# Optimization experiments

Measured on AMD Instinct MI355X. Metric: run time of the kernel, lower is better.

Reference implementation:

```python
import jax, jax.numpy as jnp
import numpy as np

B, N, K, M = 4, 32768, 128, 1024
C_IN, C_OUT, C_ATT, H = 256, 256, 256, 8
G = 32  # GroupNorm groups
EPS = 1e-6


def heat_diffusion(x, mass, evals, evecs, t):
    # to_basis: evecs^T @ (mass * x)  -> [B,K,C]
    x_spec = jnp.einsum('bnk,bnc->bkc', evecs, x * mass[..., None])
    coefs = jnp.exp(-evals[..., None] * t[None, None, :])  # [B,K,C]
    # from_basis: evecs @ spec -> [B,N,C]
    return jnp.einsum('bnk,bkc->bnc', evecs, coefs * x_spec)


def setup_inputs() -> dict:
    key = jax.random.key(0)
    ks = jax.random.split(key, 16)
    x = jax.random.normal(ks[0], (B, N, C_IN), jnp.float32)
    mass = jax.random.uniform(ks[1], (B, N), jnp.float32, 0.1, 1.0)
    evals = jnp.sort(jax.random.uniform(ks[2], (B, K), jnp.float32, 0.0, 10.0), axis=-1)
    evecs = jax.random.normal(ks[3], (B, N, K), jnp.float32) / np.sqrt(N)
    # unique sorted farthest-point indices per mesh (equiv. to boolean mask with M True)
    far_idx = jnp.stack([jnp.sort(jax.random.permutation(jax.random.fold_in(ks[4], b), N)[:M])
                         for b in range(B)]).astype(jnp.int32)
    s = 1.0 / np.sqrt(C_IN)
    params = dict(
        diff_in_t=jnp.full((C_IN,), 0.01, jnp.float32),
        diff_out_t=jnp.full((C_OUT,), 0.01, jnp.float32),
        gn_w=jnp.ones((C_IN,), jnp.float32),
        gn_b=jnp.zeros((C_IN,), jnp.float32),
        Wq=jax.random.normal(ks[5], (C_IN, C_ATT), jnp.float32) * s,
        bq=jnp.zeros((C_ATT,), jnp.float32),
        Wk=jax.random.normal(ks[6], (C_IN, C_ATT), jnp.float32) * s,
        bk=jnp.zeros((C_ATT,), jnp.float32),
        Wv=jax.random.normal(ks[7], (C_IN, C_ATT), jnp.float32) * s,
        bv=jnp.zeros((C_ATT,), jnp.float32),
        Wo=jax.random.normal(ks[8], (C_ATT, C_OUT), jnp.float32) * s,
        bo=jnp.zeros((C_OUT,), jnp.float32),
        out_w=jnp.ones((C_OUT,), jnp.float32),
    )
    return dict(x=x, mass=mass, evals=evals, evecs=evecs, far_idx=far_idx, **params)


def reference(x, mass, evals, evecs, far_idx, diff_in_t, diff_out_t, gn_w, gn_b,
              Wq, bq, Wk, bk, Wv, bv, Wo, bo, out_w):
    # clamp (torch does this in-place under no_grad)
    diff_in_t = jnp.maximum(diff_in_t, 1e-8)
    diff_out_t = jnp.maximum(diff_out_t, 1e-8)
    out_w = jnp.maximum(out_w, 1e-8)

    x = heat_diffusion(x, mass, evals, evecs, diff_in_t)  # [B,N,C_IN]

    # masked gather of farthest points -> [B,M,C_IN]
    x_far = jnp.take_along_axis(x, far_idx[..., None], axis=1)

    # GroupNorm over (group-channels, points)
    xg = x_far.reshape(B, M, G, C_IN // G)
    mu = jnp.mean(xg, axis=(1, 3), keepdims=True)
    var = jnp.var(xg, axis=(1, 3), keepdims=True)
    xg = (xg - mu) * jax.lax.rsqrt(var + EPS)
    x_far = xg.reshape(B, M, C_IN) * gn_w + gn_b

    d = C_ATT // H
    q = (x_far @ Wq + bq).reshape(B, M, H, d)
    k = (x_far @ Wk + bk).reshape(B, M, H, d)
    v = (x_far @ Wv + bv).reshape(B, M, H, d)
    scores = jnp.einsum('bqhd,bkhd->bhqk', q, k) / np.sqrt(d)
    attn = jax.nn.softmax(scores, axis=-1)
    x_far = jnp.einsum('bhqk,bkhd->bqhd', attn, v).reshape(B, M, C_ATT)
    x_far = x_far @ Wo + bo  # [B,M,C_OUT]

    # scatter back into zeros at the farthest-point rows
    z = jnp.zeros((B, N, C_OUT), x.dtype)
    z = z.at[jnp.arange(B)[:, None], far_idx].set(x_far)

    out = heat_diffusion(z, mass, evals, evecs, diff_out_t)
    return out * out_w[None, None, :]
```

## Files before the change

### kernel.cpp

```cpp
#include <hip/hip_runtime.h>
#include <hip/hip_bf16.h>


#define Bn 4
#define Nn 32768
#define Kn 128
#define Cn 256
#define Mn 1024
#define Hn 8
#define Dn 32
#define NCH 64
#define MCH 16

typedef _Float16 f16;
typedef _Float16 f16x8 __attribute__((ext_vector_type(8)));
typedef float f32x4 __attribute__((ext_vector_type(4)));
typedef unsigned int u32;
typedef unsigned int u32x4 __attribute__((ext_vector_type(4)));

__device__ __forceinline__ void gload_lds16(const float* g, float* l) {
    __builtin_amdgcn_global_load_lds(
        (const __attribute__((address_space(1))) void*)g,
        (__attribute__((address_space(3))) void*)l, 16, 0, 0);
}

static __device__ __forceinline__ u32 packf16(f16 a, f16 b) {
    union { f16 h[2]; u32 u; } x;
    x.h[0] = a; x.h[1] = b;
    return x.u;
}

__global__ __launch_bounds__(512) void k_tobasis1(
    const float* __restrict__ x, const float* __restrict__ mass,
    const float* __restrict__ evecs, float* __restrict__ part)
{
    const int nch = blockIdx.x, b = blockIdx.z;
    const int n0 = nch * (Nn / NCH);
    const int t = threadIdx.x;
    const int lane = t & 63, w = t >> 6;
    const int lr = lane & 15, lg = lane >> 4;
    const int wm = (w & 1) * 64;
    const int wc = (w >> 1) * 64;

    __shared__ __align__(16) float evS[2][32][128];
    __shared__ __align__(16) float xS[2][32][256];
    __shared__ __align__(16) f16 evT[128][64];
    __shared__ __align__(16) f16 xT[256][64];
    __shared__ __align__(16) float massS[512];

    const size_t rb0 = (size_t)b * Nn + n0;
    const float* ebase = evecs + rb0 * Kn;
    const float* xbase = x + rb0 * Cn;

    f32x4 acc[4][4] = {};

    if (w < 2) gload_lds16(mass + rb0 + w * 256 + lane * 4, massS + w * 256);
#pragma unroll
    for (int ss = 0; ss < 2; ss++) {
        const float* eb = ebase + (size_t)ss * 32 * Kn;
        const float* xb = xbase + (size_t)ss * 32 * Cn;
#pragma unroll
        for (int iw = 0; iw < 2; iw++)
            gload_lds16(eb + (w * 2 + iw) * 256 + lane * 4, &evS[ss][0][0] + (w * 2 + iw) * 256);
#pragma unroll
        for (int iw = 0; iw < 4; iw++)
            gload_lds16(xb + (w * 4 + iw) * 256 + lane * 4, &xS[ss][0][0] + (w * 4 + iw) * 256);
    }

    for (int s = 0; s < 16; s++) {
        const int p = s & 1;
        if (s == 15) { asm volatile("s_waitcnt vmcnt(0)" ::: "memory"); }
        else         { asm volatile("s_waitcnt vmcnt(6)" ::: "memory"); }
        __builtin_amdgcn_sched_barrier(0);
        __builtin_amdgcn_s_barrier();

        {
            const int k = t & 127;
            const int g = t >> 7;
            f16x8 hv, lv;
#pragma unroll
            for (int r = 0; r < 8; r++) {
                const float f = evS[p][g * 8 + r][k];
                const f16 h = (f16)f;
                hv[r] = h;
                lv[r] = (f16)(f - (float)h);
            }
            *(f16x8*)&evT[k][((g) ^ (k & 7)) * 8] = hv;
            *(f16x8*)&evT[k][((4 + g) ^ (k & 7)) * 8] = lv;
        }
        {
            const int c = t & 255;
            const int g2 = t >> 8;
#pragma unroll
            for (int jj = 0; jj < 2; jj++) {
                const int ch = g2 * 2 + jj;
                f16x8 hv, lv;
#pragma unroll
                for (int r = 0; r < 8; r++) {
                    const int n = ch * 8 + r;
                    const float f = xS[p][n][c] * massS[s * 32 + n];
                    const f16 h = (f16)f;
                    hv[r] = h;
                    lv[r] = (f16)(f - (float)h);
                }
                *(f16x8*)&xT[c][((ch) ^ (c & 7)) * 8] = hv;
                *(f16x8*)&xT[c][((4 + ch) ^ (c & 7)) * 8] = lv;
            }
        }

        asm volatile("s_waitcnt lgkmcnt(0)" ::: "memory");
        __builtin_amdgcn_sched_barrier(0);
        __builtin_amdgcn_s_barrier();

        if (s + 2 < 16) {
            const float* eb = ebase + (size_t)(s + 2) * 32 * Kn;
            const float* xb = xbase + (size_t)(s + 2) * 32 * Cn;
#pragma unroll
            for (int iw = 0; iw < 2; iw++)
                gload_lds16(eb + (w * 2 + iw) * 256 + lane * 4, &evS[p][0][0] + (w * 2 + iw) * 256);
#pragma unroll
            for (int iw = 0; iw < 4; iw++)
                gload_lds16(xb + (w * 4 + iw) * 256 + lane * 4, &xS[p][0][0] + (w * 4 + iw) * 256);
        }

        f16x8 aH[4], aL[4], bH[4], bL[4];
#pragma unroll
        for (int i = 0; i < 4; i++) {
            const int rk = wm + i * 16 + lr;
            aH[i] = *(const f16x8*)&evT[rk][((lg) ^ (rk & 7)) * 8];
            aL[i] = *(const f16x8*)&evT[rk][((4 + lg) ^ (rk & 7)) * 8];
            const int rc = wc + i * 16 + lr;
            bH[i] = *(const f16x8*)&xT[rc][((lg) ^ (rc & 7)) * 8];
            bL[i] = *(const f16x8*)&xT[rc][((4 + lg) ^ (rc & 7)) * 8];
        }
#pragma unroll
        for (int i = 0; i < 4; i++)
#pragma unroll
            for (int j = 0; j < 4; j++) {
                acc[i][j] = __builtin_amdgcn_mfma_f32_16x16x32_f16(aH[i], bH[j], acc[i][j], 0, 0, 0);
                acc[i][j] = __builtin_amdgcn_mfma_f32_16x16x32_f16(aH[i], bL[j], acc[i][j], 0, 0, 0);
                acc[i][j] = __builtin_amdgcn_mfma_f32_16x16x32_f16(aL[i], bH[j], acc[i][j], 0, 0, 0);
            }
    }

    float* dst = part + ((size_t)b * NCH + nch) * (Kn * Cn);
#pragma unroll
    for (int i = 0; i < 4; i++)
#pragma unroll
        for (int j = 0; j < 4; j++) {
            const int m0 = wm + i * 16 + lg * 4;
            const int c = wc + j * 16 + lr;
#pragma unroll
            for (int r = 0; r < 4; r++)
                dst[(size_t)(m0 + r) * Cn + c] = acc[i][j][r];
        }
}

__global__ __launch_bounds__(256) void k_reduce(
    const float* __restrict__ part, int nchunks,
    const float* __restrict__ evals, const float* __restrict__ tvec,
    float* __restrict__ spec)
{
    const int b = blockIdx.x >> 7, k = blockIdx.x & 127, c = threadIdx.x;
    float ssum = 0.f;
    const float* p = part + ((size_t)b * nchunks * Kn + k) * Cn + c;
    for (int j = 0; j < nchunks; j++) ssum += p[(size_t)j * Kn * Cn];
    const float lam = evals[b * Kn + k];
    const float tt = fmaxf(tvec[c], 1e-8f);
    spec[((size_t)b * Kn + k) * Cn + c] = ssum * __expf(-lam * tt);
}

__global__ __launch_bounds__(256) void k_spectr(
    const float* __restrict__ spec, f16* __restrict__ sTh, f16* __restrict__ sTl)
{
    const int kc = blockIdx.x, b = blockIdx.y;
    const int t = threadIdx.x;
    __shared__ f16 lh[32][258];
    __shared__ f16 ll[32][258];
#pragma unroll 8
    for (int k2 = 0; k2 < 32; k2++) {
        const float f = spec[((size_t)b * Kn + kc * 32 + k2) * Cn + t];
        const f16 h = (f16)f;
        lh[k2][t] = h;
        ll[k2][t] = (f16)(f - (float)h);
    }
    __syncthreads();
    f16x8 vh[4], vl[4];
#pragma unroll
    for (int q = 0; q < 4; q++)
#pragma unroll
        for (int j = 0; j < 8; j++) { vh[q][j] = lh[q * 8 + j][t]; vl[q][j] = ll[q * 8 + j][t]; }
    f16* dh = sTh + ((size_t)b * 256 + t) * Kn + kc * 32;
    f16* dl = sTl + ((size_t)b * 256 + t) * Kn + kc * 32;
#pragma unroll
    for (int q = 0; q < 4; q++) {
        *(f16x8*)(dh + q * 8) = vh[q];
        *(f16x8*)(dl + q * 8) = vl[q];
    }
}

__global__ __launch_bounds__(128) void k_gather(
    const float* __restrict__ evecs, const float* __restrict__ mass,
    const int* __restrict__ far, float* __restrict__ evf, float* __restrict__ massf)
{
    const int row = blockIdx.x;
    const int b = row >> 10;
    const int idx = far[row];
    const int t = threadIdx.x;
    evf[(size_t)row * Kn + t] = evecs[((size_t)b * Nn + idx) * Kn + t];
    if (t == 0) massf[row] = mass[(size_t)b * Nn + idx];
}

struct G3 {
    const float* W[3];
    const float* bias[3];
    float* out[3];
};

template<int KD, bool PERB, bool MMASS>
__global__ __launch_bounds__(256) void k_gemm64(
    const float* __restrict__ X, G3 g, const float* __restrict__ massf)
{
    const int mt = blockIdx.x, ct = blockIdx.y, z = blockIdx.z;
    const int row0 = mt * 64, c0 = ct * 64;
    const int b = row0 >> 10;
    const float* Wp = g.W[z];
    const float* bias = g.bias[z];
    float* out = g.out[z];
    const size_t woff = PERB ? (size_t)b * KD * 256 : 0;

    __shared__ float xT[32][68];
    __shared__ float wl[32][64];
    const int t = threadIdx.x, tx = t & 15, ty = t >> 4;
    float acc[4][4] = {};

    for (int k0 = 0; k0 < KD; k0 += 32) {
        {
            const int m = t >> 2, cc0 = (t & 3) * 8;
            const float* xs = X + (size_t)(row0 + m) * KD + k0 + cc0;
            float4 a0 = *(const float4*)xs, a1 = *(const float4*)(xs + 4);
            xT[cc0 + 0][m] = a0.x; xT[cc0 + 1][m] = a0.y; xT[cc0 + 2][m] = a0.z; xT[cc0 + 3][m] = a0.w;
            xT[cc0 + 4][m] = a1.x; xT[cc0 + 5][m] = a1.y; xT[cc0 + 6][m] = a1.z; xT[cc0 + 7][m] = a1.w;
        }
        {
            const int cc = t >> 3, col = (t & 7) * 8;
            const float* wsrc = Wp + woff + (size_t)(k0 + cc) * 256 + c0 + col;
            float4 a0 = *(const float4*)wsrc, a1 = *(const float4*)(wsrc + 4);
            wl[cc][col + 0] = a0.x; wl[cc][col + 1] = a0.y; wl[cc][col + 2] = a0.z; wl[cc][col + 3] = a0.w;
            wl[cc][col + 4] = a1.x; wl[cc][col + 5] = a1.y; wl[cc][col + 6] = a1.z; wl[cc][col + 7] = a1.w;
        }
        __syncthreads();
#pragma unroll 8
        for (int cc = 0; cc < 32; cc++) {
            float4 xv = *(const float4*)&xT[cc][ty * 4];
            float4 wv = *(const float4*)&wl[cc][tx * 4];
            float xa[4] = {xv.x, xv.y, xv.z, xv.w};
            float wa[4] = {wv.x, wv.y, wv.z, wv.w};
#pragma unroll
            for (int i = 0; i < 4; i++)
#pragma unroll
                for (int j = 0; j < 4; j++) acc[i][j] += xa[i] * wa[j];
        }
        __syncthreads();
    }
    float bj[4] = {0.f, 0.f, 0.f, 0.f};
    if (bias) {
#pragma unroll
        for (int j = 0; j < 4; j++) bj[j] = bias[c0 + tx * 4 + j];
    }
#pragma unroll
    for (int i = 0; i < 4; i++) {
        const int row = row0 + ty * 4 + i;
        const float mm = MMASS ? massf[row] : 1.f;
        *(float4*)(out + (size_t)row * 256 + c0 + tx * 4) =
            make_float4((acc[i][0] + bj[0]) * mm, (acc[i][1] + bj[1]) * mm,
                        (acc[i][2] + bj[2]) * mm, (acc[i][3] + bj[3]) * mm);
    }
}

__global__ __launch_bounds__(256) void k_gnstats(const float* __restrict__ xfar, float* __restrict__ gst)
{
    const int b = blockIdx.x >> 5, g = blockIdx.x & 31;
    const int t = threadIdx.x;
    float s = 0.f, s2 = 0.f;
#pragma unroll
    for (int i = 0; i < 4; i++) {
        const int m = t * 4 + i;
        const float* p = xfar + ((size_t)b * Mn + m) * Cn + g * 8;
        float4 a = *(const float4*)p;
        float4 c = *(const float4*)(p + 4);
        s += a.x + a.y + a.z + a.w + c.x + c.y + c.z + c.w;
        s2 += a.x * a.x + a.y * a.y + a.z * a.z + a.w * a.w +
              c.x * c.x + c.y * c.y + c.z * c.z + c.w * c.w;
    }
    __shared__ float sb[256], sb2[256];
    sb[t] = s; sb2[t] = s2;
    __syncthreads();
    for (int o = 128; o > 0; o >>= 1) {
        if (t < o) { sb[t] += sb[t + o]; sb2[t] += sb2[t + o]; }
        __syncthreads();
    }
    if (t == 0) {
        const float mean = sb[0] * (1.f / 8192.f);
        const float var = sb2[0] * (1.f / 8192.f) - mean * mean;
        gst[2 * blockIdx.x] = mean;
        gst[2 * blockIdx.x + 1] = rsqrtf(var + 1e-6f);
    }
}

__global__ __launch_bounds__(256) void k_gnapply(
    const float* __restrict__ xfar, const float* __restrict__ gst,
    const float* __restrict__ gw, const float* __restrict__ gb, float* __restrict__ xn)
{
    const int idx = (blockIdx.x * 256 + threadIdx.x) * 4;
    const int c = idx & 255;
    const int row = idx >> 8;
    const int b = row >> 10;
    const int g = c >> 3;
    const float2 st = *(const float2*)&gst[2 * (b * 32 + g)];
    float4 vv = *(const float4*)&xfar[idx];
    float4 w4 = *(const float4*)&gw[c];
    float4 b4 = *(const float4*)&gb[c];
    float4 o;
    o.x = (vv.x - st.x) * st.y * w4.x + b4.x;
    o.y = (vv.y - st.x) * st.y * w4.y + b4.y;
    o.z = (vv.z - st.x) * st.y * w4.z + b4.z;
    o.w = (vv.w - st.x) * st.y * w4.w + b4.w;
    *(float4*)&xn[idx] = o;
}

__global__ __launch_bounds__(256) void k_attn(
    const float* __restrict__ q, const float* __restrict__ kbuf, const float* __restrict__ vbuf,
    float* __restrict__ att)
{
    const int qt = blockIdx.x;
    const int bh = blockIdx.y;
    const int b = bh >> 3, h = bh & 7;
    const int t = threadIdx.x;
    const int lane = t & 63, w = t >> 6;
    const int lr = lane & 15, lg = lane >> 4;

    __shared__ __align__(16) f16 Kh[64][32];
    __shared__ __align__(16) f16 Kl[64][32];
    __shared__ __align__(16) f16 Vh[32][64];
    __shared__ __align__(16) f16 Vl[32][64];
    __shared__ __align__(16) u32 Pw[4][16][68];

    const size_t base = (size_t)b * Mn * Cn + h * Dn;
    const int q0 = qt * 64;

    f16x8 Qh, Ql;
    {
        const float* qp = q + base + (size_t)(q0 + w * 16 + lr) * Cn + lg * 8;
        f32x4 a0 = *(const f32x4*)qp;
        f32x4 a1 = *(const f32x4*)(qp + 4);
        const float scale = 0.17677669529663687f;
        float qv[8] = {a0[0], a0[1], a0[2], a0[3], a1[0], a1[1], a1[2], a1[3]};
#pragma unroll
        for (int r = 0; r < 8; r++) {
            const float f = qv[r] * scale;
            const f16 hh = (f16)f;
            Qh[r] = hh;
            Ql[r] = (f16)(f - (float)hh);
        }
    }

    const int krow = t >> 2, kdg = (t & 3) * 8;
    const int vrow = (t & 31) * 2, vdc = (t >> 5) * 4;

    f32x4 kr0, kr1, va, vb;
    {
        const float* kp = kbuf + base + (size_t)krow * Cn + kdg;
        kr0 = *(const f32x4*)kp; kr1 = *(const f32x4*)(kp + 4);
        const float* vp = vbuf + base + (size_t)vrow * Cn + vdc;
        va = *(const f32x4*)vp; vb = *(const f32x4*)(vp + Cn);
    }

    float m_i[4], l_i[4];
    f32x4 acc[2] = {};
#pragma unroll
    for (int r = 0; r < 4; r++) { m_i[r] = -1e30f; l_i[r] = 0.f; }

#pragma unroll 1
    for (int kt = 0; kt < 16; kt++) {
        asm volatile("" ::: "memory");
        __builtin_amdgcn_s_barrier();

        {
            float kv[8] = {kr0[0], kr0[1], kr0[2], kr0[3], kr1[0], kr1[1], kr1[2], kr1[3]};
            f16x8 hv, lv;
#pragma unroll
            for (int r = 0; r < 8; r++) {
                const f16 hh = (f16)kv[r];
                hv[r] = hh;
                lv[r] = (f16)(kv[r] - (float)hh);
            }
            *(f16x8*)&Kh[krow][kdg] = hv;
            *(f16x8*)&Kl[krow][kdg] = lv;
        }
        {
            float v0[4] = {va[0], va[1], va[2], va[3]};
            float v1[4] = {vb[0], vb[1], vb[2], vb[3]};
#pragma unroll
            for (int j = 0; j < 4; j++) {
                const int d = vdc + j;
                const f16 h0 = (f16)v0[j], h1 = (f16)v1[j];
                const f16 l0 = (f16)(v0[j] - (float)h0), l1 = (f16)(v1[j] - (float)h1);
                const int col = vrow >> 1;
                const int idx = (((col >> 2) ^ (d & 7)) << 2) | (col & 3);
                ((u32*)&Vh[d][0])[idx] = packf16(h0, h1);
                ((u32*)&Vl[d][0])[idx] = packf16(l0, l1);
            }
        }
        if (kt < 15) {
            const float* kp = kbuf + base + (size_t)((kt + 1) * 64 + krow) * Cn + kdg;
            kr0 = *(const f32x4*)kp; kr1 = *(const f32x4*)(kp + 4);
            const float* vp = vbuf + base + (size_t)((kt + 1) * 64 + vrow) * Cn + vdc;
            va = *(const f32x4*)vp; vb = *(const f32x4*)(vp + Cn);
        }

        asm volatile("s_waitcnt lgkmcnt(0)" ::: "memory");
        __builtin_amdgcn_sched_barrier(0);
        __builtin_amdgcn_s_barrier();

        f32x4 s[4];
#pragma unroll
        for (int ct = 0; ct < 4; ct++) {
            const f16x8 khi = *(const f16x8*)&Kh[ct * 16 + lr][lg * 8];
            const f16x8 klo = *(const f16x8*)&Kl[ct * 16 + lr][lg * 8];
            f32x4 z = {};
            z = __builtin_amdgcn_mfma_f32_16x16x32_f16(Qh, khi, z, 0, 0, 0);
            z = __builtin_amdgcn_mfma_f32_16x16x32_f16(Qh, klo, z, 0, 0, 0);
            z = __builtin_amdgcn_mfma_f32_16x16x32_f16(Ql, khi, z, 0, 0, 0);
            s[ct] = z;
        }

        float tm[4];
#pragma unroll
        for (int r = 0; r < 4; r++)
            tm[r] = fmaxf(fmaxf(s[0][r], s[1][r]), fmaxf(s[2][r], s[3][r]));
#pragma unroll
        for (int r = 0; r < 4; r++) {
            tm[r] = fmaxf(tm[r], __shfl_xor(tm[r], 1));
            tm[r] = fmaxf(tm[r], __shfl_xor(tm[r], 2));
            tm[r] = fmaxf(tm[r], __shfl_xor(tm[r], 4));
            tm[r] = fmaxf(tm[r], __shfl_xor(tm[r], 8));
        }
        float corr[4], rs[4];
#pragma unroll
        for (int r = 0; r < 4; r++) {
            const float nm = fmaxf(m_i[r], tm[r]);
            corr[r] = __expf(m_i[r] - nm);
            m_i[r] = nm;
            rs[r] = 0.f;
        }
#pragma unroll
        for (int ct = 0; ct < 4; ct++)
#pragma unroll
            for (int r = 0; r < 4; r++) {
                const float p = __expf(s[ct][r] - m_i[r]);
                rs[r] += p;
                const f16 ph = (f16)p;
                const f16 pl = (f16)(p - (float)ph);
                Pw[w][lg * 4 + r][ct * 16 + lr] = packf16(ph, pl);
            }
#pragma unroll
        for (int r = 0; r < 4; r++) {
            rs[r] += __shfl_xor(rs[r], 1);
            rs[r] += __shfl_xor(rs[r], 2);
            rs[r] += __shfl_xor(rs[r], 4);
            rs[r] += __shfl_xor(rs[r], 8);
            l_i[r] = l_i[r] * corr[r] + rs[r];
        }
#pragma unroll
        for (int dt = 0; dt < 2; dt++)
#pragma unroll
            for (int r = 0; r < 4; r++) acc[dt][r] *= corr[r];

        asm volatile("s_waitcnt lgkmcnt(0)" ::: "memory");
        __builtin_amdgcn_sched_barrier(0);

        f16x8 pah[2], pal[2];
#pragma unroll
        for (int kc = 0; kc < 2; kc++) {
            const u32* prow = &Pw[w][lr][0] + kc * 32 + lg * 8;
            u32x4 ua = *(const u32x4*)prow;
            u32x4 ub = *(const u32x4*)(prow + 4);
            union { u32 wd[4]; f16x8 v; } hh, ll;
            hh.wd[0] = __builtin_amdgcn_perm(ua[1], ua[0], 0x05040100u);
            hh.wd[1] = __builtin_amdgcn_perm(ua[3], ua[2], 0x05040100u);
            hh.wd[2] = __builtin_amdgcn_perm(ub[1], ub[0], 0x05040100u);
            hh.wd[3] = __builtin_amdgcn_perm(ub[3], ub[2], 0x05040100u);
            ll.wd[0] = __builtin_amdgcn_perm(ua[1], ua[0], 0x07060302u);
            ll.wd[1] = __builtin_amdgcn_perm(ua[3], ua[2], 0x07060302u);
            ll.wd[2] = __builtin_amdgcn_perm(ub[1], ub[0], 0x07060302u);
            ll.wd[3] = __builtin_amdgcn_perm(ub[3], ub[2], 0x07060302u);
            pah[kc] = hh.v;
            pal[kc] = ll.v;
        }

#pragma unroll
        for (int dt = 0; dt < 2; dt++)
#pragma unroll
            for (int kc = 0; kc < 2; kc++) {
                const int d = dt * 16 + lr;
                const int ch = ((kc * 4 + lg) ^ (lr & 7)) * 8;
                const f16x8 vh = *(const f16x8*)&Vh[d][ch];
                const f16x8 vl = *(const f16x8*)&Vl[d][ch];
                acc[dt] = __builtin_amdgcn_mfma_f32_16x16x32_f16(pah[kc], vh, acc[dt], 0, 0, 0);
                acc[dt] = __builtin_amdgcn_mfma_f32_16x16x32_f16(pah[kc], vl, acc[dt], 0, 0, 0);
                acc[dt] = __builtin_amdgcn_mfma_f32_16x16x32_f16(pal[kc], vh, acc[dt], 0, 0, 0);
            }
    }

#pragma unroll
    for (int r = 0; r < 4; r++) {
        const float inv = 1.f / l_i[r];
        const size_t orow = (size_t)b * Mn + q0 + w * 16 + lg * 4 + r;
#pragma unroll
        for (int dt = 0; dt < 2; dt++)
            att[orow * Cn + h * Dn + dt * 16 + lr] = acc[dt][r] * inv;
    }
}

__global__ __launch_bounds__(256) void k_tobasis2(
    const float* __restrict__ evf, const float* __restrict__ xo, float* __restrict__ part)
{
    const int mch = blockIdx.x, ct = blockIdx.y, b = blockIdx.z;
    const int m0 = mch * (Mn / MCH);
    const int c0 = ct * 128;
    __shared__ float ev[32][128];
    __shared__ float xm[32][128];
    const int t = threadIdx.x, tx = t & 15, ty = t >> 4;
    float acc[8][8];
#pragma unroll
    for (int i = 0; i < 8; i++)
#pragma unroll
        for (int j = 0; j < 8; j++) acc[i][j] = 0.f;
    const int lr = t >> 3, lc = (t & 7) * 16;
    for (int s = 0; s < Mn / MCH; s += 32) {
        const size_t mrow = (size_t)b * Mn + m0 + s + lr;
        {
            const float* es = evf + mrow * Kn + lc;
            *(float4*)&ev[lr][lc]      = *(const float4*)es;
            *(float4*)&ev[lr][lc + 4]  = *(const float4*)(es + 4);
            *(float4*)&ev[lr][lc + 8]  = *(const float4*)(es + 8);
            *(float4*)&ev[lr][lc + 12] = *(const float4*)(es + 12);
            const float* xs = xo + mrow * Cn + c0 + lc;
            *(float4*)&xm[lr][lc]      = *(const float4*)xs;
            *(float4*)&xm[lr][lc + 4]  = *(const float4*)(xs + 4);
            *(float4*)&xm[lr][lc + 8]  = *(const float4*)(xs + 8);
            *(float4*)&xm[lr][lc + 12] = *(const float4*)(xs + 12);
        }
        __syncthreads();
#pragma unroll 4
        for (int nn = 0; nn < 32; nn++) {
            float4 e0 = *(const float4*)&ev[nn][ty * 4];
            float4 e1 = *(const float4*)&ev[nn][64 + ty * 4];
            float4 x0 = *(const float4*)&xm[nn][tx * 4];
            float4 x1 = *(const float4*)&xm[nn][64 + tx * 4];
            float ee[8] = {e0.x, e0.y, e0.z, e0.w, e1.x, e1.y, e1.z, e1.w};
            float xx[8] = {x0.x, x0.y, x0.z, x0.w, x1.x, x1.y, x1.z, x1.w};
#pragma unroll
            for (int i = 0; i < 8; i++)
#pragma unroll
                for (int j = 0; j < 8; j++) acc[i][j] += ee[i] * xx[j];
        }
        __syncthreads();
    }
    float* dst = part + ((size_t)b * MCH + mch) * (Kn * Cn);
#pragma unroll
    for (int i = 0; i < 8; i++) {
        const int k = (i < 4) ? (ty * 4 + i) : (64 + ty * 4 + i - 4);
        *(float4*)(dst + (size_t)k * Cn + c0 + tx * 4) =
            make_float4(acc[i][0], acc[i][1], acc[i][2], acc[i][3]);
        *(float4*)(dst + (size_t)k * Cn + c0 + 64 + tx * 4) =
            make_float4(acc[i][4], acc[i][5], acc[i][6], acc[i][7]);
    }
}

__global__ __launch_bounds__(512) void k_frombasis2(
    const float* __restrict__ evecs, const f16* __restrict__ sTh,
    const f16* __restrict__ sTl, const float* __restrict__ outw,
    float* __restrict__ out)
{
    const int nt = blockIdx.x, b = blockIdx.z;
    const int n0 = nt * 128;
    const int t = threadIdx.x;
    const int lane = t & 63, w = t >> 6;
    const int lr = lane & 15, lg = lane >> 4;
    const int wn = (w & 1) * 64;
    const int wc = (w >> 1) * 64;

    __shared__ __align__(16) f16 aT[2][128][64];

    const int srow = t >> 2;
    const int skc = t & 3;
    const float* Abase = evecs + ((size_t)b * Nn + n0 + srow) * Kn + skc * 8;

    const f16* Bh = sTh + ((size_t)b * 256 + wc + lr) * Kn + lg * 8;
    const f16* Bl = sTl + ((size_t)b * 256 + wc + lr) * Kn + lg * 8;

    f32x4 acc[4][4] = {};

    f32x4 a0 = *(const f32x4*)(Abase);
    f32x4 a1 = *(const f32x4*)(Abase + 4);

#pragma unroll 1
    for (int kk = 0; kk < 4; kk++) {
        const int p = kk & 1;
        {
            float av[8] = {a0[0], a0[1], a0[2], a0[3], a1[0], a1[1], a1[2], a1[3]};
            f16x8 hv, lv;
#pragma unroll
            for (int r = 0; r < 8; r++) {
                const float f = av[r] * 256.f;
                const f16 hh = (f16)f;
                hv[r] = hh;
                lv[r] = (f16)(f - (float)hh);
            }
            *(f16x8*)&aT[p][srow][((skc) ^ (srow & 7)) * 8] = hv;
            *(f16x8*)&aT[p][srow][((4 + skc) ^ (srow & 7)) * 8] = lv;
        }
        if (kk < 3) {
            a0 = *(const f32x4*)(Abase + (kk + 1) * 32);
            a1 = *(const f32x4*)(Abase + (kk + 1) * 32 + 4);
        }
        f16x8 bh[4], bl[4];
#pragma unroll
        for (int cf = 0; cf < 4; cf++) {
            bh[cf] = *(const f16x8*)(Bh + (size_t)cf * 16 * Kn + kk * 32);
            bl[cf] = *(const f16x8*)(Bl + (size_t)cf * 16 * Kn + kk * 32);
        }

        asm volatile("s_waitcnt lgkmcnt(0)" ::: "memory");
        __builtin_amdgcn_sched_barrier(0);
        __builtin_amdgcn_s_barrier();

#pragma unroll
        for (int rf = 0; rf < 4; rf++) {
            const int rn = wn + rf * 16 + lr;
            const f16x8 ah = *(const f16x8*)&aT[p][rn][((lg) ^ (rn & 7)) * 8];
            const f16x8 al = *(const f16x8*)&aT[p][rn][((4 + lg) ^ (rn & 7)) * 8];
#pragma unroll
            for (int cf = 0; cf < 4; cf++) {
                acc[rf][cf] = __builtin_amdgcn_mfma_f32_16x16x32_f16(ah, bh[cf], acc[rf][cf], 0, 0, 0);
                acc[rf][cf] = __builtin_amdgcn_mfma_f32_16x16x32_f16(ah, bl[cf], acc[rf][cf], 0, 0, 0);
                acc[rf][cf] = __builtin_amdgcn_mfma_f32_16x16x32_f16(al, bh[cf], acc[rf][cf], 0, 0, 0);
            }
        }
    }

    float ow4[4];
#pragma unroll
    for (int cf = 0; cf < 4; cf++)
        ow4[cf] = fmaxf(outw[wc + cf * 16 + lr], 1e-8f) * (1.f / 256.f);
#pragma unroll
    for (int rf = 0; rf < 4; rf++)
#pragma unroll
        for (int cf = 0; cf < 4; cf++) {
            const int nn = n0 + wn + rf * 16 + lg * 4;
            const int c = wc + cf * 16 + lr;
#pragma unroll
            for (int r = 0; r < 4; r++)
                out[((size_t)b * Nn + nn + r) * Cn + c] = acc[rf][cf][r] * ow4[cf];
        }
}

extern "C" void kernel_launch(void* const* d_in, const int* in_sizes, int n_in,
                              void* d_out, int out_size, void* d_ws, size_t ws_size,
                              hipStream_t stream)
{
    const float* x     = (const float*)d_in[0];
    const float* mass  = (const float*)d_in[1];
    const float* evals = (const float*)d_in[2];
    const float* evecs = (const float*)d_in[3];
    const int*   far   = (const int*)d_in[4];
    const float* t_in  = (const float*)d_in[5];
    const float* t_out = (const float*)d_in[6];
    const float* gn_w  = (const float*)d_in[7];
    const float* gn_b  = (const float*)d_in[8];
    const float* Wq    = (const float*)d_in[9];
    const float* bq    = (const float*)d_in[10];
    const float* Wk    = (const float*)d_in[11];
    const float* bk    = (const float*)d_in[12];
    const float* Wv    = (const float*)d_in[13];
    const float* bv    = (const float*)d_in[14];
    const float* Wo    = (const float*)d_in[15];
    const float* bo    = (const float*)d_in[16];
    const float* outw  = (const float*)d_in[17];
    float* out = (float*)d_out;
    float* ws = (float*)d_ws;

    float* A     = ws;
    float* evf   = ws    + 8388608;
    float* massf = evf   + 524288;
    float* gst   = massf + 4096;
    float* pm    = gst   + 256;
    float* pl    = pm    + 262144;
    float* spec1 = pl    + 262144;
    float* xfar  = spec1 + 131072;
    float* xn    = xfar  + 1048576;
    float* q     = xn    + 1048576;
    float* kk    = q     + 1048576;
    float* v     = kk    + 1048576;
    float* part2 = A;
    float* spec2 = spec1;
    float* xo    = xfar;
    float* att   = xn;
    f16* specTh  = (f16*)pm;
    f16* specTl  = specTh + 131072;
    (void)pl;

    k_tobasis1<<<dim3(NCH, 1, Bn), 512, 0, stream>>>(x, mass, evecs, A);
    k_reduce<<<Bn * Kn, Cn, 0, stream>>>(A, NCH, evals, t_in, spec1);
    k_gather<<<Bn * Mn, Kn, 0, stream>>>(evecs, mass, far, evf, massf);
    {
        G3 g{};
        g.W[0] = spec1; g.bias[0] = nullptr; g.out[0] = xfar;
        k_gemm64<128, true, false><<<dim3(64, 4, 1), 256, 0, stream>>>(evf, g, nullptr);
    }
    k_gnstats<<<Bn * 32, 256, 0, stream>>>(xfar, gst);
    k_gnapply<<<1024, 256, 0, stream>>>(xfar, gst, gn_w, gn_b, xn);
    {
        G3 g{};
        g.W[0] = Wq; g.W[1] = Wk; g.W[2] = Wv;
        g.bias[0] = bq; g.bias[1] = bk; g.bias[2] = bv;
        g.out[0] = q; g.out[1] = kk; g.out[2] = v;
        k_gemm64<256, false, false><<<dim3(64, 4, 3), 256, 0, stream>>>(xn, g, nullptr);
    }
    k_attn<<<dim3(16, 32), 256, 0, stream>>>(q, kk, v, att);
    {
        G3 g{};
        g.W[0] = Wo; g.bias[0] = bo; g.out[0] = xo;
        k_gemm64<256, false, true><<<dim3(64, 4, 1), 256, 0, stream>>>(att, g, massf);
    }
    k_tobasis2<<<dim3(MCH, 2, Bn), 256, 0, stream>>>(evf, xo, part2);
    k_reduce<<<Bn * Kn, Cn, 0, stream>>>(part2, MCH, evals, t_out, spec2);
    k_spectr<<<dim3(4, Bn), 256, 0, stream>>>(spec2, specTh, specTl);
    k_frombasis2<<<dim3(256, 1, Bn), 512, 0, stream>>>(evecs, specTh, specTl, outw, out);
}
```

Baseline: 506.2 us.

## Load x tile to registers in tobasis kernel, single-buffer evecs to raise occupancy

The first to-basis kernel no longer stages x and mass through LDS with double buffering. It loads them straight into registers for the next chunk, writes packed f16 pairs into the transposed tile using a new swizzle, and keeps only a single evecs LDS buffer. Launch bounds now request 4 blocks per SM to use the reduced LDS footprint. The cost is losing the two-deep prefetch: the loop now waits on vmcnt(0) every iteration, so load latency may be exposed, and register pressure rises.

```diff
diff --git a/kernel.cpp b/kernel.cpp
--- a/kernel.cpp
+++ b/kernel.cpp
@@ -15,6 +15,7 @@
 typedef _Float16 f16;
 typedef _Float16 f16x8 __attribute__((ext_vector_type(8)));
 typedef float f32x4 __attribute__((ext_vector_type(4)));
+typedef float f32x2 __attribute__((ext_vector_type(2)));
 typedef unsigned int u32;
 typedef unsigned int u32x4 __attribute__((ext_vector_type(4)));
 
@@ -30,7 +31,7 @@
     return x.u;
 }
 
-__global__ __launch_bounds__(512) void k_tobasis1(
+__global__ __launch_bounds__(512, 4) void k_tobasis1(
     const float* __restrict__ x, const float* __restrict__ mass,
     const float* __restrict__ evecs, float* __restrict__ part)
 {
@@ -42,35 +43,33 @@
     const int wm = (w & 1) * 64;
     const int wc = (w >> 1) * 64;
 
-    __shared__ __align__(16) float evS[2][32][128];
-    __shared__ __align__(16) float xS[2][32][256];
+    __shared__ __align__(16) float evS[32][128];
     __shared__ __align__(16) f16 evT[128][64];
     __shared__ __align__(16) f16 xT[256][64];
-    __shared__ __align__(16) float massS[512];
 
     const size_t rb0 = (size_t)b * Nn + n0;
     const float* ebase = evecs + rb0 * Kn;
     const float* xbase = x + rb0 * Cn;
+    const float* mbase = mass + rb0;
+
+    const int cc = t & 31, np = t >> 5;
 
     f32x4 acc[4][4] = {};
 
-    if (w < 2) gload_lds16(mass + rb0 + w * 256 + lane * 4, massS + w * 256);
-#pragma unroll
-    for (int ss = 0; ss < 2; ss++) {
-        const float* eb = ebase + (size_t)ss * 32 * Kn;
-        const float* xb = xbase + (size_t)ss * 32 * Cn;
-#pragma unroll
-        for (int iw = 0; iw < 2; iw++)
-            gload_lds16(eb + (w * 2 + iw) * 256 + lane * 4, &evS[ss][0][0] + (w * 2 + iw) * 256);
-#pragma unroll
-        for (int iw = 0; iw < 4; iw++)
-            gload_lds16(xb + (w * 4 + iw) * 256 + lane * 4, &xS[ss][0][0] + (w * 4 + iw) * 256);
+#pragma unroll
+    for (int iw = 0; iw < 2; iw++)
+        gload_lds16(ebase + (w * 2 + iw) * 256 + lane * 4, &evS[0][0] + (w * 2 + iw) * 256);
+    f32x4 xa0, xa1, xb0, xb1;
+    f32x2 mreg;
+    {
+        const float* xp = xbase + (size_t)(np * 2) * Cn + cc * 8;
+        xa0 = *(const f32x4*)xp;       xa1 = *(const f32x4*)(xp + 4);
+        xb0 = *(const f32x4*)(xp + Cn); xb1 = *(const f32x4*)(xp + Cn + 4);
+        mreg = *(const f32x2*)(mbase + np * 2);
     }
 
     for (int s = 0; s < 16; s++) {
-        const int p = s & 1;
-        if (s == 15) { asm volatile("s_waitcnt vmcnt(0)" ::: "memory"); }
-        else         { asm volatile("s_waitcnt vmcnt(6)" ::: "memory"); }
+        asm volatile("s_waitcnt vmcnt(0)" ::: "memory");
         __builtin_amdgcn_sched_barrier(0);
         __builtin_amdgcn_s_barrier();
 
@@ -80,7 +79,7 @@
             f16x8 hv, lv;
 #pragma unroll
             for (int r = 0; r < 8; r++) {
-                const float f = evS[p][g * 8 + r][k];
+                const float f = evS[g * 8 + r][k];
                 const f16 h = (f16)f;
                 hv[r] = h;
                 lv[r] = (f16)(f - (float)h);
@@ -89,22 +88,20 @@
             *(f16x8*)&evT[k][((4 + g) ^ (k & 7)) * 8] = lv;
         }
         {
-            const int c = t & 255;
-            const int g2 = t >> 8;
-#pragma unroll
-            for (int jj = 0; jj < 2; jj++) {
-                const int ch = g2 * 2 + jj;
-                f16x8 hv, lv;
-#pragma unroll
-                for (int r = 0; r < 8; r++) {
-                    const int n = ch * 8 + r;
-                    const float f = xS[p][n][c] * massS[s * 32 + n];
-                    const f16 h = (f16)f;
-                    hv[r] = h;
-                    lv[r] = (f16)(f - (float)h);
-                }
-                *(f16x8*)&xT[c][((ch) ^ (c & 7)) * 8] = hv;
-                *(f16x8*)&xT[c][((4 + ch) ^ (c & 7)) * 8] = lv;
+            const float m0 = mreg[0], m1 = mreg[1];
+            float r0[8] = {xa0[0]*m0, xa0[1]*m0, xa0[2]*m0, xa0[3]*m0,
+                           xa1[0]*m0, xa1[1]*m0, xa1[2]*m0, xa1[3]*m0};
+            float r1[8] = {xb0[0]*m1, xb0[1]*m1, xb0[2]*m1, xb0[3]*m1,
+                           xb1[0]*m1, xb1[1]*m1, xb1[2]*m1, xb1[3]*m1};
+#pragma unroll
+            for (int j = 0; j < 8; j++) {
+                const int c = cc * 8 + j;
+                const int g = (c >> 3) & 7;
+                const f16 h0 = (f16)r0[j], h1 = (f16)r1[j];
+                const f16 l0 = (f16)(r0[j] - (float)h0), l1 = (f16)(r1[j] - (float)h1);
+                u32* row = (u32*)&xT[c][0];
+                row[((((np >> 2)    ) ^ g) << 2) | (np & 3)] = packf16(h0, h1);
+                row[((((np >> 2) + 4) ^ g) << 2) | (np & 3)] = packf16(l0, l1);
             }
         }
 
@@ -112,15 +109,15 @@
         __builtin_amdgcn_sched_barrier(0);
         __builtin_amdgcn_s_barrier();
 
-        if (s + 2 < 16) {
-            const float* eb = ebase + (size_t)(s + 2) * 32 * Kn;
-            const float* xb = xbase + (size_t)(s + 2) * 32 * Cn;
+        if (s < 15) {
+            const float* eb = ebase + (size_t)(s + 1) * 32 * Kn;
 #pragma unroll
             for (int iw = 0; iw < 2; iw++)
-                gload_lds16(eb + (w * 2 + iw) * 256 + lane * 4, &evS[p][0][0] + (w * 2 + iw) * 256);
-#pragma unroll
-            for (int iw = 0; iw < 4; iw++)
-                gload_lds16(xb + (w * 4 + iw) * 256 + lane * 4, &xS[p][0][0] + (w * 4 + iw) * 256);
+                gload_lds16(eb + (w * 2 + iw) * 256 + lane * 4, &evS[0][0] + (w * 2 + iw) * 256);
+            const float* xp = xbase + (size_t)((s + 1) * 32 + np * 2) * Cn + cc * 8;
+            xa0 = *(const f32x4*)xp;       xa1 = *(const f32x4*)(xp + 4);
+            xb0 = *(const f32x4*)(xp + Cn); xb1 = *(const f32x4*)(xp + Cn + 4);
+            mreg = *(const f32x2*)(mbase + (s + 1) * 32 + np * 2);
         }
 
         f16x8 aH[4], aL[4], bH[4], bL[4];
@@ -130,8 +127,9 @@
             aH[i] = *(const f16x8*)&evT[rk][((lg) ^ (rk & 7)) * 8];
             aL[i] = *(const f16x8*)&evT[rk][((4 + lg) ^ (rk & 7)) * 8];
             const int rc = wc + i * 16 + lr;
-            bH[i] = *(const f16x8*)&xT[rc][((lg) ^ (rc & 7)) * 8];
-            bL[i] = *(const f16x8*)&xT[rc][((4 + lg) ^ (rc & 7)) * 8];
+            const int gg = (rc >> 3) & 7;
+            bH[i] = *(const f16x8*)&xT[rc][((lg) ^ gg) * 8];
+            bL[i] = *(const f16x8*)&xT[rc][((4 + lg) ^ gg) * 8];
         }
 #pragma unroll
         for (int i = 0; i < 4; i++)
```

After: 504.0 us. No clear change (-0.4%).
